# Kernel tuning notes

Measured on AMD Instinct MI355X. Metric: run time of the kernel, lower is better.

The kernel has to match this reference:

```python
import jax, jax.numpy as jnp
import numpy as np

B, M, P, W = 128, 10000, 64, 24


def setup_inputs() -> dict:
    key = jax.random.key(0)
    k1, k2, k3 = jax.random.split(key, 3)
    x = jax.random.normal(k1, (B, M, P), dtype=jnp.float32)
    weight = jax.random.normal(k2, (M, P, W), dtype=jnp.float32)
    bound = 1.0 / np.sqrt(P)
    bias = jax.random.uniform(k3, (M, W), dtype=jnp.float32, minval=-bound, maxval=bound)
    return {"x": x, "weight": weight, "bias": bias}


def reference(x, weight, bias):
    # Per-channel linear: out[b, w, j] = sum_p x[b, j, p] * weight[j, p, w] + bias[j, w]
    # Replaces the original python loop of m tiny GEMMs with one batched contraction.
    out = jnp.einsum('bjp,jpw->bwj', x, weight) + bias.T[None, :, :]  # [B, W, M]
    return out
```

## Files before the change

kernel.cpp:

```cpp
#include <hip/hip_runtime.h>


constexpr int B  = 128;
constexpr int M  = 10000;
constexpr int P  = 64;
constexpr int W  = 24;

constexpr int JT  = 16;
constexpr int BH  = 16;
constexpr int NCH = 4;
constexpr int NT  = 512;
constexpr int NWG = (M / JT) * (B / (BH * NCH));

using bf8   = __attribute__((ext_vector_type(8))) __bf16;
using f32x4 = __attribute__((ext_vector_type(4))) float;

__device__ __forceinline__ unsigned short rne_bf16(float f) {
  const unsigned u = __float_as_uint(f);
  return (unsigned short)((u + 0x7fffu + ((u >> 16) & 1u)) >> 16);
}

__global__ __launch_bounds__(NT, 4) void pcl_kernel(
    const float* __restrict__ x, const float* __restrict__ wgt,
    const float* __restrict__ bias, float* __restrict__ out) {
  __shared__ __align__(16) char smem[81920];
  unsigned short* wsh  = reinterpret_cast<unsigned short*>(smem);
  unsigned short* xsh  = reinterpret_cast<unsigned short*>(smem + 49152);
  float*          obuf = reinterpret_cast<float*>(smem + 49152);

  const int t = threadIdx.x;

  const int orig = blockIdx.x;
  const int xcd  = orig & 7;
  const int idx  = orig >> 3;
  const int wgid = (xcd < 2 ? xcd * 157 : 314 + (xcd - 2) * 156) + idx;
  const int jt    = wgid >> 1;
  const int bbase = (wgid & 1) * (BH * NCH);
  const int j0    = jt * JT;

  const int wk   = t >> 6;
  const int lane = t & 63;
  const int col  = lane & 15;
  const int kg   = lane >> 4;

  float bv[2][2];
#pragma unroll
  for (int jj = 0; jj < 2; ++jj) {
    const int j = j0 + wk + 8 * jj;
#pragma unroll
    for (int nt = 0; nt < 2; ++nt) {
      const int w = nt * 16 + col;
      bv[jj][nt] = (w < W) ? bias[(size_t)j * W + w] : 0.0f;
    }
  }

  float4 nx[8];
#pragma unroll
  for (int i = 0; i < 8; ++i) {
    const int g   = t + i * NT;
    const int b   = g >> 8;
    const int j   = (g >> 4) & 15;
    const int c2  = g & 15;
    nx[i] = *reinterpret_cast<const float4*>(
        x + ((size_t)(bbase + b) * M + j0 + j) * P + 4 * c2);
  }

  {
    const float4* wg4 = reinterpret_cast<const float4*>(wgt);
#pragma unroll
    for (int i = 0; i < 12; ++i) {
      const int s  = t + i * NT;
      const int j  = s / 384;
      const int rr = s - j * 384;
      const int p  = rr / 6;
      const int w4 = (rr - 6 * p) * 4;
      const float4 v = wg4[(size_t)(j0 + j) * 384 + rr];
      const float vv[4] = {v.x, v.y, v.z, v.w};
#pragma unroll
      for (int k = 0; k < 4; ++k) {
        const int w = w4 + k;
        wsh[((j * W + w) << 6) + (((p >> 3) ^ (w & 7)) << 3) + (p & 7)] =
            rne_bf16(vv[k]);
      }
    }
  }

  for (int c = 0; c < NCH; ++c) {
    if (c > 0) __syncthreads();

#pragma unroll
    for (int i = 0; i < 8; ++i) {
      const int g  = t + i * NT;
      const int b  = g >> 8;
      const int j  = (g >> 4) & 15;
      const int c2 = g & 15;
      const unsigned u0 =
          (unsigned)rne_bf16(nx[i].x) | ((unsigned)rne_bf16(nx[i].y) << 16);
      const unsigned u1 =
          (unsigned)rne_bf16(nx[i].z) | ((unsigned)rne_bf16(nx[i].w) << 16);
      const int s = (c2 >> 1) ^ (b & 7);
      *reinterpret_cast<uint2*>(xsh + (((b << 4) + j) << 6) + (s << 3) +
                                ((c2 & 1) << 2)) = uint2{u0, u1};
    }

    if (c < NCH - 1) {
      const int b0n = bbase + (c + 1) * BH;
#pragma unroll
      for (int i = 0; i < 8; ++i) {
        const int g   = t + i * NT;
        const int b   = g >> 8;
        const int j   = (g >> 4) & 15;
        const int c2  = g & 15;
        nx[i] = *reinterpret_cast<const float4*>(
            x + ((size_t)(b0n + b) * M + j0 + j) * P + 4 * c2);
      }
    }

    __syncthreads();

    f32x4 acc[2][2];
#pragma unroll
    for (int jj = 0; jj < 2; ++jj)
#pragma unroll
      for (int nt = 0; nt < 2; ++nt)
        acc[jj][nt] = f32x4{bv[jj][nt], bv[jj][nt], bv[jj][nt], bv[jj][nt]};

#pragma unroll
    for (int jj = 0; jj < 2; ++jj) {
      const int jl = wk + 8 * jj;
#pragma unroll
      for (int ks = 0; ks < 2; ++ks) {
        const int cc = ks * 4 + kg;
        const bf8 af = *reinterpret_cast<const bf8*>(
            xsh + (((col << 4) + jl) << 6) + ((cc ^ (col & 7)) << 3));
        bf8 bfr[2];
#pragma unroll
        for (int nt = 0; nt < 2; ++nt) {
          const int w  = nt * 16 + col;
          const int wr = (w < W) ? w : 0;
          bf8 v = *reinterpret_cast<const bf8*>(
              wsh + ((jl * W + wr) << 6) + ((cc ^ (wr & 7)) << 3));
          if (w >= W) {
#pragma unroll
            for (int e = 0; e < 8; ++e) v[e] = (__bf16)0.0f;
          }
          bfr[nt] = v;
        }
#pragma unroll
        for (int nt = 0; nt < 2; ++nt)
          acc[jj][nt] = __builtin_amdgcn_mfma_f32_16x16x32_bf16(
              af, bfr[nt], acc[jj][nt], 0, 0, 0);
      }
    }

    __syncthreads();

#pragma unroll
    for (int jj = 0; jj < 2; ++jj) {
      const int jl = wk + 8 * jj;
#pragma unroll
      for (int nt = 0; nt < 2; ++nt) {
        const int w = nt * 16 + col;
        if (w < W) {
#pragma unroll
          for (int reg = 0; reg < 4; ++reg)
            obuf[(jl * 16 + kg * 4 + reg) * 25 + w] = acc[jj][nt][reg];
        }
      }
    }
    __syncthreads();

    const int b0c = bbase + c * BH;
#pragma unroll
    for (int it = 0; it < 3; ++it) {
      const int d    = t + it * NT;
      const int jq   = d & 3;
      const int rest = d >> 2;
      const int w    = rest % 24;
      const int br   = rest / 24;
      float4 o;
      o.x = obuf[((4 * jq + 0) * 16 + br) * 25 + w];
      o.y = obuf[((4 * jq + 1) * 16 + br) * 25 + w];
      o.z = obuf[((4 * jq + 2) * 16 + br) * 25 + w];
      o.w = obuf[((4 * jq + 3) * 16 + br) * 25 + w];
      *reinterpret_cast<float4*>(
          out + ((size_t)(b0c + br) * W + w) * M + j0 + 4 * jq) = o;
    }
  }
}

extern "C" void kernel_launch(void* const* d_in, const int* in_sizes, int n_in,
                              void* d_out, int out_size, void* d_ws, size_t ws_size,
                              hipStream_t stream) {
  const float* x    = (const float*)d_in[0];
  const float* wgt  = (const float*)d_in[1];
  const float* bias = (const float*)d_in[2];
  float* out        = (float*)d_out;

  dim3 grid(NWG);
  dim3 block(NT);
  hipLaunchKernelGGL(pcl_kernel, grid, block, 0, stream, x, wgt, bias, out);
}
```

Measured before the change: 119.6 us.

## Keep weight fragments in registers and double threads per workgroup

Each of 16 waves now owns one channel j. Each wave loads its bf16 weight fragments straight from global memory into registers with strided scalar loads, instead of staging the weight tile through LDS. Shared memory drops from 80KB to 32KB and the block grows to 1024 threads, so each thread prefetches fewer x vectors. Bf16 conversion now uses native casts. The weight loads are strided 4-byte gathers, stride W, which may coalesce poorly, and __launch_bounds__(1024,4) may not be satisfiable.

After: 111.7 us (median of 2 runs). 1.07x faster.

```diff
diff --git a/kernel.cpp b/kernel.cpp
--- a/kernel.cpp
+++ b/kernel.cpp
@@ -9,24 +9,19 @@
 constexpr int JT  = 16;
 constexpr int BH  = 16;
 constexpr int NCH = 4;
-constexpr int NT  = 512;
+constexpr int NT  = 1024;
 constexpr int NWG = (M / JT) * (B / (BH * NCH));
 
 using bf8   = __attribute__((ext_vector_type(8))) __bf16;
+using bf4   = __attribute__((ext_vector_type(4))) __bf16;
 using f32x4 = __attribute__((ext_vector_type(4))) float;
-
-__device__ __forceinline__ unsigned short rne_bf16(float f) {
-  const unsigned u = __float_as_uint(f);
-  return (unsigned short)((u + 0x7fffu + ((u >> 16) & 1u)) >> 16);
-}
 
 __global__ __launch_bounds__(NT, 4) void pcl_kernel(
     const float* __restrict__ x, const float* __restrict__ wgt,
     const float* __restrict__ bias, float* __restrict__ out) {
-  __shared__ __align__(16) char smem[81920];
-  unsigned short* wsh  = reinterpret_cast<unsigned short*>(smem);
-  unsigned short* xsh  = reinterpret_cast<unsigned short*>(smem + 49152);
-  float*          obuf = reinterpret_cast<float*>(smem + 49152);
+  __shared__ __align__(16) char smem[32768];
+  unsigned short* xsh  = reinterpret_cast<unsigned short*>(smem);
+  float*          obuf = reinterpret_cast<float*>(smem);
 
   const int t = threadIdx.x;
 
@@ -42,149 +37,124 @@
   const int lane = t & 63;
   const int col  = lane & 15;
   const int kg   = lane >> 4;
+  const int j    = j0 + wk;
 
-  float bv[2][2];
+  float bv[2];
 #pragma unroll
-  for (int jj = 0; jj < 2; ++jj) {
-    const int j = j0 + wk + 8 * jj;
+  for (int nt = 0; nt < 2; ++nt) {
+    const int w = nt * 16 + col;
+    bv[nt] = (w < W) ? bias[(size_t)j * W + w] : 0.0f;
+  }
+
+  bf8 bfr[2][2];
+#pragma unroll
+  for (int ks = 0; ks < 2; ++ks) {
 #pragma unroll
     for (int nt = 0; nt < 2; ++nt) {
-      const int w = nt * 16 + col;
-      bv[jj][nt] = (w < W) ? bias[(size_t)j * W + w] : 0.0f;
+      const int w     = nt * 16 + col;
+      const bool ok   = (w < W);
+      const float* wp = wgt + (size_t)j * (P * W) +
+                        (size_t)(ks * 32 + kg * 8) * W + (ok ? w : 0);
+      bf8 v;
+#pragma unroll
+      for (int e = 0; e < 8; ++e) v[e] = (__bf16)wp[(size_t)e * W];
+      if (!ok) {
+#pragma unroll
+        for (int e = 0; e < 8; ++e) v[e] = (__bf16)0.0f;
+      }
+      bfr[ks][nt] = v;
     }
   }
 
-  float4 nx[8];
+  float4 nx[4];
 #pragma unroll
-  for (int i = 0; i < 8; ++i) {
-    const int g   = t + i * NT;
-    const int b   = g >> 8;
-    const int j   = (g >> 4) & 15;
-    const int c2  = g & 15;
+  for (int i = 0; i < 4; ++i) {
+    const int g  = t + i * NT;
+    const int b  = g >> 8;
+    const int jj = (g >> 4) & 15;
+    const int c2 = g & 15;
     nx[i] = *reinterpret_cast<const float4*>(
-        x + ((size_t)(bbase + b) * M + j0 + j) * P + 4 * c2);
-  }
-
-  {
-    const float4* wg4 = reinterpret_cast<const float4*>(wgt);
-#pragma unroll
-    for (int i = 0; i < 12; ++i) {
-      const int s  = t + i * NT;
-      const int j  = s / 384;
-      const int rr = s - j * 384;
-      const int p  = rr / 6;
-      const int w4 = (rr - 6 * p) * 4;
-      const float4 v = wg4[(size_t)(j0 + j) * 384 + rr];
-      const float vv[4] = {v.x, v.y, v.z, v.w};
-#pragma unroll
-      for (int k = 0; k < 4; ++k) {
-        const int w = w4 + k;
-        wsh[((j * W + w) << 6) + (((p >> 3) ^ (w & 7)) << 3) + (p & 7)] =
-            rne_bf16(vv[k]);
-      }
-    }
+        x + ((size_t)(bbase + b) * M + j0 + jj) * P + 4 * c2);
   }
 
   for (int c = 0; c < NCH; ++c) {
     if (c > 0) __syncthreads();
 
 #pragma unroll
-    for (int i = 0; i < 8; ++i) {
+    for (int i = 0; i < 4; ++i) {
       const int g  = t + i * NT;
       const int b  = g >> 8;
-      const int j  = (g >> 4) & 15;
+      const int jj = (g >> 4) & 15;
       const int c2 = g & 15;
-      const unsigned u0 =
-          (unsigned)rne_bf16(nx[i].x) | ((unsigned)rne_bf16(nx[i].y) << 16);
-      const unsigned u1 =
-          (unsigned)rne_bf16(nx[i].z) | ((unsigned)rne_bf16(nx[i].w) << 16);
+      bf4 v;
+      v[0] = (__bf16)nx[i].x; v[1] = (__bf16)nx[i].y;
+      v[2] = (__bf16)nx[i].z; v[3] = (__bf16)nx[i].w;
       const int s = (c2 >> 1) ^ (b & 7);
-      *reinterpret_cast<uint2*>(xsh + (((b << 4) + j) << 6) + (s << 3) +
-                                ((c2 & 1) << 2)) = uint2{u0, u1};
+      *reinterpret_cast<bf4*>(xsh + (((b << 4) + jj) << 6) + (s << 3) +
+                              ((c2 & 1) << 2)) = v;
     }
 
     if (c < NCH - 1) {
       const int b0n = bbase + (c + 1) * BH;
 #pragma unroll
-      for (int i = 0; i < 8; ++i) {
-        const int g   = t + i * NT;
-        const int b   = g >> 8;
-        const int j   = (g >> 4) & 15;
-        const int c2  = g & 15;
+      for (int i = 0; i < 4; ++i) {
+        const int g  = t + i * NT;
+        const int b  = g >> 8;
+        const int jj = (g >> 4) & 15;
+        const int c2 = g & 15;
         nx[i] = *reinterpret_cast<const float4*>(
-            x + ((size_t)(b0n + b) * M + j0 + j) * P + 4 * c2);
+            x + ((size_t)(b0n + b) * M + j0 + jj) * P + 4 * c2);
       }
     }
 
     __syncthreads();
 
-    f32x4 acc[2][2];
+    f32x4 acc[2];
 #pragma unroll
-    for (int jj = 0; jj < 2; ++jj)
+    for (int nt = 0; nt < 2; ++nt)
+      acc[nt] = f32x4{bv[nt], bv[nt], bv[nt], bv[nt]};
+
+#pragma unroll
+    for (int ks = 0; ks < 2; ++ks) {
+      const int cc = ks * 4 + kg;
+      const bf8 af = *reinterpret_cast<const bf8*>(
+          xsh + (((col << 4) + wk) << 6) + ((cc ^ (col & 7)) << 3));
 #pragma unroll
       for (int nt = 0; nt < 2; ++nt)
-        acc[jj][nt] = f32x4{bv[jj][nt], bv[jj][nt], bv[jj][nt], bv[jj][nt]};
-
-#pragma unroll
-    for (int jj = 0; jj < 2; ++jj) {
-      const int jl = wk + 8 * jj;
-#pragma unroll
-      for (int ks = 0; ks < 2; ++ks) {
-        const int cc = ks * 4 + kg;
-        const bf8 af = *reinterpret_cast<const bf8*>(
-            xsh + (((col << 4) + jl) << 6) + ((cc ^ (col & 7)) << 3));
-        bf8 bfr[2];
-#pragma unroll
-        for (int nt = 0; nt < 2; ++nt) {
-          const int w  = nt * 16 + col;
-          const int wr = (w < W) ? w : 0;
-          bf8 v = *reinterpret_cast<const bf8*>(
-              wsh + ((jl * W + wr) << 6) + ((cc ^ (wr & 7)) << 3));
-          if (w >= W) {
-#pragma unroll
-            for (int e = 0; e < 8; ++e) v[e] = (__bf16)0.0f;
-          }
-          bfr[nt] = v;
-        }
-#pragma unroll
-        for (int nt = 0; nt < 2; ++nt)
-          acc[jj][nt] = __builtin_amdgcn_mfma_f32_16x16x32_bf16(
-              af, bfr[nt], acc[jj][nt], 0, 0, 0);
-      }
+        acc[nt] = __builtin_amdgcn_mfma_f32_16x16x32_bf16(
+            af, bfr[ks][nt], acc[nt], 0, 0, 0);
     }
 
     __syncthreads();
 
 #pragma unroll
-    for (int jj = 0; jj < 2; ++jj) {
-      const int jl = wk + 8 * jj;
+    for (int nt = 0; nt < 2; ++nt) {
+      const int w = nt * 16 + col;
+      if (w < W) {
 #pragma unroll
-      for (int nt = 0; nt < 2; ++nt) {
-        const int w = nt * 16 + col;
-        if (w < W) {
-#pragma unroll
-          for (int reg = 0; reg < 4; ++reg)
-            obuf[(jl * 16 + kg * 4 + reg) * 25 + w] = acc[jj][nt][reg];
-        }
+        for (int reg = 0; reg < 4; ++reg)
+          obuf[(wk * 16 + kg * 4 + reg) * 25 + w] = acc[nt][reg];
       }
     }
     __syncthreads();
 
     const int b0c = bbase + c * BH;
 #pragma unroll
-    for (int it = 0; it < 3; ++it) {
-      const int d    = t + it * NT;
-      const int jq   = d & 3;
-      const int rest = d >> 2;
-      const int w    = rest % 24;
-      const int br   = rest / 24;
-      float4 o;
-      o.x = obuf[((4 * jq + 0) * 16 + br) * 25 + w];
-      o.y = obuf[((4 * jq + 1) * 16 + br) * 25 + w];
-      o.z = obuf[((4 * jq + 2) * 16 + br) * 25 + w];
-      o.w = obuf[((4 * jq + 3) * 16 + br) * 25 + w];
-      *reinterpret_cast<float4*>(
-          out + ((size_t)(b0c + br) * W + w) * M + j0 + 4 * jq) = o;
+    for (int it = 0; it < 2; ++it) {
+      const int d = t + it * NT;
+      if (d < 1536) {
+        const int jq   = d & 3;
+        const int rest = d >> 2;
+        const int w    = rest % 24;
+        const int br   = rest / 24;
+        float4 o;
+        o.x = obuf[((4 * jq + 0) * 16 + br) * 25 + w];
+        o.y = obuf[((4 * jq + 1) * 16 + br) * 25 + w];
+        o.z = obuf[((4 * jq + 2) * 16 + br) * 25 + w];
+        o.w = obuf[((4 * jq + 3) * 16 + br) * 25 + w];
+        *reinterpret_cast<float4*>(
+            out + ((size_t)(b0c + br) * W + w) * M + j0 + 4 * jq) = o;
+      }
     }
   }
 }
```
